# Kernel tuning notes

Hardware: AMD Instinct MI355X
Metric: run time of the kernel (lower is better)

The kernel has to match this reference:

```python
import jax, jax.numpy as jnp
import numpy as np

B_GRAPHS = 32
EMB = 512
ESM = 1280
HEADS = 8
HEAD_DIM = EMB // HEADS


def _segments():
    lengths = 256 + 8 * np.arange(B_GRAPHS)          # 256..504, N = 12160
    batch_ids = np.repeat(np.arange(B_GRAPHS), lengths).astype(np.int32)
    pos = np.concatenate([np.arange(l) for l in lengths]).astype(np.int32)
    return batch_ids, pos, int(lengths.max()), int(lengths.sum())


def setup_inputs() -> dict:
    key = jax.random.key(0)
    ks = jax.random.split(key, 10)
    batch_ids, pos, pad_len, n = _segments()
    s = 0.02
    return {
        "esm_embedding": jax.random.normal(ks[0], (n, ESM), jnp.float32),
        "h": jax.random.normal(ks[1], (n, EMB), jnp.float32),
        "W_esm": jax.random.normal(ks[2], (EMB, ESM), jnp.float32) * s,
        "b_esm": jnp.zeros((EMB,), jnp.float32),
        "Wq": jax.random.normal(ks[3], (EMB, EMB), jnp.float32) * s,
        "bq": jnp.zeros((EMB,), jnp.float32),
        "Wk": jax.random.normal(ks[4], (EMB, EMB), jnp.float32) * s,
        "bk": jnp.zeros((EMB,), jnp.float32),
        "Wv": jax.random.normal(ks[5], (EMB, EMB), jnp.float32) * s,
        "bv": jnp.zeros((EMB,), jnp.float32),
        "Wo": jax.random.normal(ks[6], (EMB, EMB), jnp.float32) * s,
        "bo": jnp.zeros((EMB,), jnp.float32),
        "gamma": jnp.ones((EMB,), jnp.float32),
        "beta": jnp.zeros((EMB,), jnp.float32),
        "batch_ids": jnp.asarray(batch_ids),
        "pos": jnp.asarray(pos),
        "pad_len": pad_len,
        "num_graphs": B_GRAPHS,
    }


def _layer_norm(x, gamma, beta, eps=1e-5):
    mu = jnp.mean(x, axis=-1, keepdims=True)
    var = jnp.var(x, axis=-1, keepdims=True)
    return (x - mu) * jax.lax.rsqrt(var + eps) * gamma + beta


def reference(esm_embedding, h, W_esm, b_esm, Wq, bq, Wk, bk, Wv, bv, Wo, bo,
              gamma, beta, batch_ids, pos, pad_len, num_graphs):
    B, P, D, H, hd = num_graphs, pad_len, EMB, HEADS, HEAD_DIM
    residual = h
    # to_dense_batch: scatter nodes into [B, P, *] padded tensors + key mask
    h_dense = jnp.zeros((B, P, D), h.dtype).at[batch_ids, pos].set(h)
    h_mask = jnp.zeros((B, P), bool).at[batch_ids, pos].set(True)
    h_esm = esm_embedding @ W_esm.T + b_esm                      # [N, D]
    esm_dense = jnp.zeros((B, P, D), h.dtype).at[batch_ids, pos].set(h_esm)

    q = (h_dense @ Wq.T + bq).reshape(B, P, H, hd)
    k = (esm_dense @ Wk.T + bk).reshape(B, P, H, hd)
    v = (esm_dense @ Wv.T + bv).reshape(B, P, H, hd)

    scores = jnp.einsum("bqhd,bkhd->bhqk", q, k) / jnp.sqrt(jnp.float32(hd))
    scores = jnp.where(h_mask[:, None, None, :], scores, -jnp.inf)
    attn = jax.nn.softmax(scores, axis=-1)                        # [B,H,P,P]
    out = jnp.einsum("bhqk,bkhd->bqhd", attn, v).reshape(B, P, D)
    out = out @ Wo.T + bo
    out = out[batch_ids, pos]                                     # unpad -> [N, D]
    return _layer_norm(out + residual, gamma, beta)
```

## Files before the change

### kernel.cpp

```cpp
#include <hip/hip_runtime.h>

#define NTOT 12160
#define EMBD 512
#define ESMD 1280
#define NHEAD 8
#define HD 64
#define NG 32
#define NTILE 768

typedef __attribute__((ext_vector_type(8))) short short8v;
typedef __attribute__((ext_vector_type(4))) short short4v;
typedef __attribute__((ext_vector_type(4))) float floatx4;

__device__ inline short f2bf(float f) {
  union { float f; unsigned u; } v; v.f = f;
  unsigned r = v.u + 0x7fffu + ((v.u >> 16) & 1u);
  return (short)(r >> 16);
}

__device__ inline void gload_lds16(const void* g, void* l) {
  __builtin_amdgcn_global_load_lds((const __attribute__((address_space(1))) void*)g,
                                   (__attribute__((address_space(3))) void*)l, 16, 0, 0);
}

__device__ inline int node_graph(int n) {
  int g = (int)((sqrtf(3969.f + (float)n) - 63.f) * 0.5f);
  if (4 * (g + 1) * (g + 64) <= n) g++;
  else if (4 * g * (g + 63) > n) g--;
  return g;
}

__global__ __launch_bounds__(256) void cvt_kernel(
    const float* __restrict__ esm, const float* __restrict__ Wq,
    const float* __restrict__ Wk, const float* __restrict__ Wv,
    const float* __restrict__ Wo,
    short* __restrict__ esm_b, short* __restrict__ Wq_b,
    short* __restrict__ Wk_b, short* __restrict__ Wv_b, short* __restrict__ Wo_b)
{
  int idx = blockIdx.x * 256 + threadIdx.x;
  const float* src; short* dst; int off;
  if      (idx < 3891200) { src = esm; dst = esm_b; off = idx; }
  else if (idx < 3956736) { src = Wq;  dst = Wq_b;  off = idx - 3891200; }
  else if (idx < 4022272) { src = Wk;  dst = Wk_b;  off = idx - 3956736; }
  else if (idx < 4087808) { src = Wv;  dst = Wv_b;  off = idx - 4022272; }
  else                    { src = Wo;  dst = Wo_b;  off = idx - 4087808; }
  const float4 v = *(const float4*)&src[(size_t)off * 4];
  short4v s; s[0] = f2bf(v.x); s[1] = f2bf(v.y); s[2] = f2bf(v.z); s[3] = f2bf(v.w);
  *(short4v*)&dst[(size_t)off * 4] = s;
}

__global__ __launch_bounds__(256) void wtrans_kernel(
    const float* __restrict__ W, short* __restrict__ WT)
{
  __shared__ short t[32][33];
  const int c0 = blockIdx.x * 32;
  const int r0 = blockIdx.y * 32;
  const int tr = threadIdx.x >> 5, tc = threadIdx.x & 31;
  for (int i = 0; i < 4; i++)
    t[i * 8 + tr][tc] = f2bf(W[(size_t)(r0 + i * 8 + tr) * 1280 + c0 + tc]);
  __syncthreads();
  for (int i = 0; i < 4; i++)
    WT[(size_t)(c0 + i * 8 + tr) * 512 + r0 + tc] = t[tc][i * 8 + tr];
}

__global__ __launch_bounds__(256) void bfuse_kernel(
    const float* __restrict__ Wk, const float* __restrict__ Wv,
    const float* __restrict__ besm, const float* __restrict__ bk,
    const float* __restrict__ bv, float* __restrict__ bkp, float* __restrict__ bvp)
{
  int wgid = blockIdx.x * 4 + (threadIdx.x >> 6);
  int lane = threadIdx.x & 63;
  const float* W  = (wgid < 512) ? Wk : Wv;
  const float* ba = (wgid < 512) ? bk : bv;
  float* o        = (wgid < 512) ? bkp : bvp;
  int row = wgid & 511;
  const float4 w0 = *(const float4*)&W[(size_t)row * 512 + lane * 8];
  const float4 w1 = *(const float4*)&W[(size_t)row * 512 + lane * 8 + 4];
  const float4 b0 = *(const float4*)&besm[lane * 8];
  const float4 b1 = *(const float4*)&besm[lane * 8 + 4];
  float s = w0.x * b0.x + w0.y * b0.y + w0.z * b0.z + w0.w * b0.w
          + w1.x * b1.x + w1.y * b1.y + w1.z * b1.z + w1.w * b1.w;
  for (int off = 1; off < 64; off <<= 1) s += __shfl_xor(s, off);
  if (lane == 0) o[row] = s + ba[row];
}

template<int AF32>
__device__ inline void gemm_core(const void* __restrict__ Ap, const short* __restrict__ W,
                                 int K, int row0, int col0,
                                 short* As, short* Bs, floatx4 acc[4][4])
{
  const int tid = threadIdx.x;
  const int lane = tid & 63, wave = tid >> 6;
  const int l15 = lane & 15, quad = lane >> 4;
  const int wm = (wave >> 1) * 64, wn = (wave & 1) * 64;
  const int lrow = lane >> 3;
  const int scol = ((lane & 7) ^ lrow) * 8;
  const int swz = l15 & 7;

  for (int k0 = 0; k0 < K; k0 += 64) {
    if (k0) __syncthreads();
    if (AF32) {
      const float* A = (const float*)Ap;
      for (int p = 0; p < 8; p++) {
        int idx = p * 256 + tid;
        int r = idx >> 4, c4 = idx & 15;
        const float4 v = *(const float4*)&A[(size_t)(row0 + r) * K + k0 + c4 * 4];
        short4v sv; sv[0] = f2bf(v.x); sv[1] = f2bf(v.y); sv[2] = f2bf(v.z); sv[3] = f2bf(v.w);
        *(short4v*)&As[r * 64 + (((c4 >> 1) ^ (r & 7)) << 3) + ((c4 & 1) << 2)] = sv;
      }
    } else {
      const short* A = (const short*)Ap;
      for (int p = 0; p < 4; p++) {
        int seg = wave * 4 + p;
        gload_lds16(&A[(size_t)(row0 + seg * 8 + lrow) * K + k0 + scol], &As[seg * 512]);
      }
    }
    for (int p = 0; p < 4; p++) {
      int seg = wave * 4 + p;
      gload_lds16(&W[(size_t)(col0 + seg * 8 + lrow) * K + k0 + scol], &Bs[seg * 512]);
    }
    __syncthreads();
    for (int ks = 0; ks < 64; ks += 32) {
      const int off = (((ks >> 3) + quad) ^ swz) << 3;
      short8v a[4], b[4];
      for (int mt = 0; mt < 4; mt++)
        a[mt] = *(const short8v*)&As[(wm + mt * 16 + l15) * 64 + off];
      for (int nt = 0; nt < 4; nt++)
        b[nt] = *(const short8v*)&Bs[(wn + nt * 16 + l15) * 64 + off];
      for (int mt = 0; mt < 4; mt++)
        for (int nt = 0; nt < 4; nt++)
          acc[mt][nt] = __builtin_amdgcn_mfma_f32_16x16x32_bf16(a[mt], b[nt], acc[mt][nt], 0, 0, 0);
    }
  }
}

__device__ inline void epi_bf16(floatx4 acc[4][4], const float* bias, short* C,
                                int row0, int col0, int wm, int wn, int l15, int quad)
{
  for (int nt = 0; nt < 4; nt++) {
    int col = col0 + wn + nt * 16 + l15;
    float bv = bias[col];
    for (int mt = 0; mt < 4; mt++) {
      int rowb = row0 + wm + mt * 16 + quad * 4;
      for (int r = 0; r < 4; r++)
        C[(size_t)(rowb + r) * EMBD + col] = f2bf(acc[mt][nt][r] + bv);
    }
  }
}

__global__ __launch_bounds__(256) void wfuse_gemm(
    const short* __restrict__ Wk_b, const short* __restrict__ Wv_b,
    const short* __restrict__ WT, short* __restrict__ Wkp, short* __restrict__ Wvp)
{
  __shared__ short As[128 * 64];
  __shared__ short Bs[128 * 64];
  const int wh = blockIdx.x >= 10;
  const int col0 = (blockIdx.x - (wh ? 10 : 0)) * 128;
  const int row0 = blockIdx.y * 128;
  floatx4 acc[4][4];
  for (int i = 0; i < 4; i++) for (int j = 0; j < 4; j++)
    for (int r = 0; r < 4; r++) acc[i][j][r] = 0.f;
  gemm_core<0>(wh ? Wv_b : Wk_b, WT, 512, row0, col0, As, Bs, acc);
  short* O = wh ? Wvp : Wkp;
  const int lane = threadIdx.x & 63, wave = threadIdx.x >> 6;
  const int l15 = lane & 15, quad = lane >> 4;
  const int wm = (wave >> 1) * 64, wn = (wave & 1) * 64;
  for (int nt = 0; nt < 4; nt++) {
    int col = col0 + wn + nt * 16 + l15;
    for (int mt = 0; mt < 4; mt++) {
      int rowb = row0 + wm + mt * 16 + quad * 4;
      for (int r = 0; r < 4; r++)
        O[(size_t)(rowb + r) * ESMD + col] = f2bf(acc[mt][nt][r]);
    }
  }
}

__global__ __launch_bounds__(256) void qkv_gemm(
    const float* __restrict__ hf, const short* __restrict__ esm_b,
    const short* __restrict__ Wq_b, const short* __restrict__ Wkp, const short* __restrict__ Wvp,
    const float* __restrict__ bq, const float* __restrict__ bkp, const float* __restrict__ bvp,
    short* __restrict__ qb, short* __restrict__ kp, short* __restrict__ vp)
{
  __shared__ short As[128 * 64];
  __shared__ short Bs[128 * 64];
  const int which = blockIdx.x >> 2;
  const int row0 = blockIdx.y * 128, col0 = (blockIdx.x & 3) * 128;
  floatx4 acc[4][4];
  for (int i = 0; i < 4; i++) for (int j = 0; j < 4; j++)
    for (int r = 0; r < 4; r++) acc[i][j][r] = 0.f;
  if (which == 0) gemm_core<1>(hf,    Wq_b, 512,  row0, col0, As, Bs, acc);
  else if (which == 1) gemm_core<0>(esm_b, Wkp, 1280, row0, col0, As, Bs, acc);
  else gemm_core<0>(esm_b, Wvp, 1280, row0, col0, As, Bs, acc);

  const int lane = threadIdx.x & 63, wave = threadIdx.x >> 6;
  const int l15 = lane & 15, quad = lane >> 4;
  const int wm = (wave >> 1) * 64, wn = (wave & 1) * 64;

  if (which == 0) {
    epi_bf16(acc, bq, qb, row0, col0, wm, wn, l15, quad);
  } else if (which == 1) {
    for (int mt = 0; mt < 4; mt++) {
      int rowb = row0 + wm + mt * 16 + quad * 4;
      int g = node_graph(rowb);
      int loc = rowb - 4 * g * (g + 63);
      int ptile = 16 * g + (g * g) / 4 + (loc >> 4);
      int l15k = loc & 15;
      for (int nt = 0; nt < 4; nt++) {
        int col = col0 + wn + nt * 16 + l15;
        float bv = bkp[col];
        int hh = col >> 6, dh = col & 63;
        int hfh = dh >> 5, qk = (dh & 31) >> 3, jk = dh & 7;
        size_t base = ((size_t)(hh * NTILE + ptile) * 2 + hfh) * 512
                      + (size_t)l15k * 32 + qk * 8 + jk;
        for (int r = 0; r < 4; r++)
          kp[base + (size_t)r * 32] = f2bf(acc[mt][nt][r] + bv);
      }
    }
  } else {
    for (int mt = 0; mt < 4; mt++) {
      int rowb = row0 + wm + mt * 16 + quad * 4;
      int g = node_graph(rowb);
      int loc = rowb - 4 * g * (g + 63);
      int ptile = 16 * g + (g * g) / 4 + (loc >> 4);
      int koff = loc & 15;
      for (int nt = 0; nt < 4; nt++) {
        int col = col0 + wn + nt * 16 + l15;
        float bv = bvp[col];
        int hh = col >> 6, dh = col & 63;
        int dt = dh >> 4, l15v = dh & 15;
        size_t base = ((size_t)(hh * 4 + dt) * NTILE + ptile) * 256
                      + (size_t)l15v * 16 + koff;
        short4v sv;
        for (int r = 0; r < 4; r++) sv[r] = f2bf(acc[mt][nt][r] + bv);
        *(short4v*)&vp[base] = sv;
      }
    }
  }
}

template<bool MASK>
__device__ inline void attn_chunk(
    int kc, int L, int Tg, int hb, int hdt4,
    const short* __restrict__ kp, const short* __restrict__ vp,
    short* Ps, const short8v& aq0, const short8v& aq1,
    floatx4 oacc[4], float rowsum[4], int l15, int quad)
{
  floatx4 s[4];
  const int t0 = Tg + (kc >> 4);
  for (int sub = 0; sub < 4; sub++) {
    const short* kpt = &kp[((size_t)(hb + t0 + sub) * 2) * 512 + l15 * 32 + quad * 8];
    short8v b0 = *(const short8v*)kpt;
    short8v b1 = *(const short8v*)(kpt + 512);
    floatx4 c; for (int r = 0; r < 4; r++) c[r] = 0.f;
    c = __builtin_amdgcn_mfma_f32_16x16x32_bf16(aq0, b0, c, 0, 0, 0);
    c = __builtin_amdgcn_mfma_f32_16x16x32_bf16(aq1, b1, c, 0, 0, 0);
    s[sub] = c;
  }
  for (int sub = 0; sub < 4; sub++)
    for (int r = 0; r < 4; r++) {
      float p = __expf(s[sub][r] * 0.125f);
      if (MASK && (kc + sub * 16 + l15 >= L)) p = 0.f;
      rowsum[r] += p;
      Ps[(quad * 4 + r) * 72 + sub * 16 + l15] = f2bf(p);
    }
  for (int half = 0; half < 2; half++) {
    short8v pA = *(const short8v*)&Ps[l15 * 72 + half * 32 + quad * 8];
    for (int dt = 0; dt < 4; dt++) {
      size_t vbase = ((size_t)(hdt4 + dt) * NTILE + t0 + half * 2 + (quad >> 1)) * 256
                     + (size_t)l15 * 16 + (quad & 1) * 8;
      short8v bvv = *(const short8v*)&vp[vbase];
      oacc[dt] = __builtin_amdgcn_mfma_f32_16x16x32_bf16(pA, bvv, oacc[dt], 0, 0, 0);
    }
  }
}

__global__ __launch_bounds__(512) void attn_kernel(
    const short* __restrict__ qb, const short* __restrict__ kp,
    const short* __restrict__ vp, short* __restrict__ ao)
{
  __shared__ short Ps_all[8][16 * 72];
  const int x = blockIdx.x & 7, j = blockIdx.x >> 3;
  int g = -1, qt = 0, accum = 0;
  for (int i = 0; i < 4; i++) {
    int gg = x + 8 * i;
    int t = 16 + ((gg + 1) >> 1);
    if (j < accum + t) { g = gg; qt = j - accum; break; }
    accum += t;
  }
  if (g < 0) return;
  const int L = 256 + 8 * g;
  const int start = 4 * g * (g + 63);
  const int Tg = 16 * g + (g * g) / 4;
  const int h = threadIdx.x >> 6;
  const int lane = threadIdx.x & 63;
  const int l15 = lane & 15, quad = lane >> 4;
  const int hb = h * NTILE, hdt4 = h * 4;
  short* Ps = Ps_all[h];

  int qrow = qt * 16 + l15;
  if (qrow > L - 1) qrow = L - 1;
  const size_t qoff = (size_t)(start + qrow) * EMBD + h * HD + quad * 8;
  const short8v aq0 = *(const short8v*)&qb[qoff];
  const short8v aq1 = *(const short8v*)&qb[qoff + 32];

  float rowsum[4];
  floatx4 oacc[4];
  for (int r = 0; r < 4; r++) rowsum[r] = 0.f;
  for (int dt = 0; dt < 4; dt++)
    for (int r = 0; r < 4; r++) oacc[dt][r] = 0.f;

  const int Lfull = L & ~63;
  for (int kc = 0; kc < Lfull; kc += 64)
    attn_chunk<false>(kc, L, Tg, hb, hdt4, kp, vp, Ps, aq0, aq1, oacc, rowsum, l15, quad);
  if (Lfull < L)
    attn_chunk<true>(Lfull, L, Tg, hb, hdt4, kp, vp, Ps, aq0, aq1, oacc, rowsum, l15, quad);

  float inv[4];
  for (int r = 0; r < 4; r++) {
    float red = rowsum[r];
    red += __shfl_xor(red, 1); red += __shfl_xor(red, 2);
    red += __shfl_xor(red, 4); red += __shfl_xor(red, 8);
    inv[r] = 1.f / red;
  }
  for (int dt = 0; dt < 4; dt++)
    for (int r = 0; r < 4; r++) {
      int rl = qt * 16 + quad * 4 + r;
      if (rl < L)
        ao[(size_t)(start + rl) * EMBD + h * HD + dt * 16 + l15] = f2bf(oacc[dt][r] * inv[r]);
    }
}

__global__ __launch_bounds__(256) void o_gemm(
    const short* __restrict__ A, const short* __restrict__ W,
    const float* __restrict__ bias, float* __restrict__ C)
{
  __shared__ short As[128 * 64];
  __shared__ short Bs[128 * 64];
  floatx4 acc[4][4];
  for (int i = 0; i < 4; i++) for (int j = 0; j < 4; j++)
    for (int r = 0; r < 4; r++) acc[i][j][r] = 0.f;
  const int row0 = blockIdx.y * 128, col0 = blockIdx.x * 128;
  gemm_core<0>(A, W, EMBD, row0, col0, As, Bs, acc);
  const int lane = threadIdx.x & 63, wave = threadIdx.x >> 6;
  const int l15 = lane & 15, quad = lane >> 4;
  const int wm = (wave >> 1) * 64, wn = (wave & 1) * 64;
  for (int nt = 0; nt < 4; nt++) {
    int col = col0 + wn + nt * 16 + l15;
    float bv = bias[col];
    for (int mt = 0; mt < 4; mt++) {
      int rowb = row0 + wm + mt * 16 + quad * 4;
      for (int r = 0; r < 4; r++)
        C[(size_t)(rowb + r) * EMBD + col] = acc[mt][nt][r] + bv;
    }
  }
}

__global__ __launch_bounds__(64) void ln_kernel(
    float* __restrict__ y, const float* __restrict__ hres,
    const float* __restrict__ gamma, const float* __restrict__ beta)
{
  const int row = blockIdx.x;
  const int lane = threadIdx.x;
  const size_t base = (size_t)row * EMBD + lane * 8;
  const float4 a0 = *(const float4*)&y[base];
  const float4 a1 = *(const float4*)&y[base + 4];
  const float4 b0 = *(const float4*)&hres[base];
  const float4 b1 = *(const float4*)&hres[base + 4];
  float x[8] = { a0.x + b0.x, a0.y + b0.y, a0.z + b0.z, a0.w + b0.w,
                 a1.x + b1.x, a1.y + b1.y, a1.z + b1.z, a1.w + b1.w };
  float s = 0.f, s2 = 0.f;
  for (int i = 0; i < 8; i++) { s += x[i]; s2 += x[i] * x[i]; }
  for (int off = 1; off < 64; off <<= 1) { s += __shfl_xor(s, off); s2 += __shfl_xor(s2, off); }
  const float mu = s * (1.f / 512.f);
  const float var = s2 * (1.f / 512.f) - mu * mu;
  const float rstd = rsqrtf(var + 1e-5f);
  const float4 g0 = *(const float4*)&gamma[lane * 8];
  const float4 g1 = *(const float4*)&gamma[lane * 8 + 4];
  const float4 e0 = *(const float4*)&beta[lane * 8];
  const float4 e1 = *(const float4*)&beta[lane * 8 + 4];
  const float gg[8] = { g0.x, g0.y, g0.z, g0.w, g1.x, g1.y, g1.z, g1.w };
  const float ee[8] = { e0.x, e0.y, e0.z, e0.w, e1.x, e1.y, e1.z, e1.w };
  float o[8];
  for (int i = 0; i < 8; i++) o[i] = (x[i] - mu) * rstd * gg[i] + ee[i];
  *(float4*)&y[base]     = make_float4(o[0], o[1], o[2], o[3]);
  *(float4*)&y[base + 4] = make_float4(o[4], o[5], o[6], o[7]);
}

extern "C" void kernel_launch(void* const* d_in, const int* in_sizes, int n_in,
                              void* d_out, int out_size, void* d_ws, size_t ws_size,
                              hipStream_t stream)
{
  (void)in_sizes; (void)n_in; (void)out_size; (void)ws_size;
  const float* esm   = (const float*)d_in[0];
  const float* h     = (const float*)d_in[1];
  const float* Wesm  = (const float*)d_in[2];
  const float* besm  = (const float*)d_in[3];
  const float* Wq    = (const float*)d_in[4];
  const float* bq    = (const float*)d_in[5];
  const float* Wk    = (const float*)d_in[6];
  const float* bk    = (const float*)d_in[7];
  const float* Wv    = (const float*)d_in[8];
  const float* bv    = (const float*)d_in[9];
  const float* Wo    = (const float*)d_in[10];
  const float* bo    = (const float*)d_in[11];
  const float* gamma = (const float*)d_in[12];
  const float* beta  = (const float*)d_in[13];

  char* ws = (char*)d_ws;
  short* esm_b  = (short*)ws;
  short* ao     = esm_b;
  short* kp     = (short*)(ws + 31129600);
  short* WesmT  = kp;
  short* vp     = (short*)(ws + 43712512);
  short* Wq_b   = (short*)(ws + 56295424);
  short* Wk_b   = (short*)(ws + 56819712);
  short* Wv_b   = (short*)(ws + 57344000);
  short* Wo_b   = (short*)(ws + 57868288);
  short* Wkp    = (short*)(ws + 58392576);
  short* Wvp    = (short*)(ws + 59703296);
  float* bkp    = (float*)(ws + 61014016);
  float* bvp    = (float*)(ws + 61016064);
  short* qb     = (short*)d_out;
  float* y      = (float*)d_out;

  cvt_kernel<<<dim3(16224), dim3(256), 0, stream>>>(
      esm, Wq, Wk, Wv, Wo, esm_b, Wq_b, Wk_b, Wv_b, Wo_b);
  wtrans_kernel<<<dim3(40, 16), dim3(256), 0, stream>>>(Wesm, WesmT);
  bfuse_kernel<<<dim3(256), dim3(256), 0, stream>>>(Wk, Wv, besm, bk, bv, bkp, bvp);
  wfuse_gemm<<<dim3(20, 4), dim3(256), 0, stream>>>(Wk_b, Wv_b, WesmT, Wkp, Wvp);
  qkv_gemm<<<dim3(12, 95), dim3(256), 0, stream>>>(
      h, esm_b, Wq_b, Wkp, Wvp, bq, bkp, bvp, qb, kp, vp);
  attn_kernel<<<dim3(832), dim3(512), 0, stream>>>(qb, kp, vp, ao);
  o_gemm<<<dim3(4, 95), dim3(256), 0, stream>>>(ao, Wo_b, bo, y);
  ln_kernel<<<dim3(NTOT), dim3(64), 0, stream>>>(y, h, gamma, beta);
}
```

Measured before the change: 306.6 us.

## Widen QKV GEMM tile to 128x256, pre-convert h to bf16, XCD-aware block mapping

The h input is converted to bf16 in the bulk conversion kernel and written into spare space in the output buffer, so the QKV GEMM loads both operands through direct global-to-LDS copies instead of an fp32 load-convert path. The QKV GEMM becomes a 512-thread block with a 128x256 output tile, which halves the number of times each A row tile is re-read. A 1D grid is remapped so that blocks sharing a row tile land on the same XCD, to improve L2 reuse of A. The trade-offs are an extra conversion pass over h, a larger LDS footprint per block, and some idle blocks past the last row tile.

```diff
diff --git a/kernel.cpp b/kernel.cpp
--- a/kernel.cpp
+++ b/kernel.cpp
@@ -31,19 +31,20 @@
 }
 
 __global__ __launch_bounds__(256) void cvt_kernel(
-    const float* __restrict__ esm, const float* __restrict__ Wq,
-    const float* __restrict__ Wk, const float* __restrict__ Wv,
-    const float* __restrict__ Wo,
-    short* __restrict__ esm_b, short* __restrict__ Wq_b,
+    const float* __restrict__ esm, const float* __restrict__ h,
+    const float* __restrict__ Wq, const float* __restrict__ Wk,
+    const float* __restrict__ Wv, const float* __restrict__ Wo,
+    short* __restrict__ esm_b, short* __restrict__ h_b, short* __restrict__ Wq_b,
     short* __restrict__ Wk_b, short* __restrict__ Wv_b, short* __restrict__ Wo_b)
 {
   int idx = blockIdx.x * 256 + threadIdx.x;
   const float* src; short* dst; int off;
   if      (idx < 3891200) { src = esm; dst = esm_b; off = idx; }
-  else if (idx < 3956736) { src = Wq;  dst = Wq_b;  off = idx - 3891200; }
-  else if (idx < 4022272) { src = Wk;  dst = Wk_b;  off = idx - 3956736; }
-  else if (idx < 4087808) { src = Wv;  dst = Wv_b;  off = idx - 4022272; }
-  else                    { src = Wo;  dst = Wo_b;  off = idx - 4087808; }
+  else if (idx < 5447680) { src = h;   dst = h_b;   off = idx - 3891200; }
+  else if (idx < 5513216) { src = Wq;  dst = Wq_b;  off = idx - 5447680; }
+  else if (idx < 5578752) { src = Wk;  dst = Wk_b;  off = idx - 5513216; }
+  else if (idx < 5644288) { src = Wv;  dst = Wv_b;  off = idx - 5578752; }
+  else                    { src = Wo;  dst = Wo_b;  off = idx - 5644288; }
   const float4 v = *(const float4*)&src[(size_t)off * 4];
   short4v s; s[0] = f2bf(v.x); s[1] = f2bf(v.y); s[2] = f2bf(v.z); s[3] = f2bf(v.w);
   *(short4v*)&dst[(size_t)off * 4] = s;
@@ -84,8 +85,7 @@
   if (lane == 0) o[row] = s + ba[row];
 }
 
-template<int AF32>
-__device__ inline void gemm_core(const void* __restrict__ Ap, const short* __restrict__ W,
+__device__ inline void gemm_core(const short* __restrict__ A, const short* __restrict__ W,
                                  int K, int row0, int col0,
                                  short* As, short* Bs, floatx4 acc[4][4])
 {
@@ -99,21 +99,9 @@
 
   for (int k0 = 0; k0 < K; k0 += 64) {
     if (k0) __syncthreads();
-    if (AF32) {
-      const float* A = (const float*)Ap;
-      for (int p = 0; p < 8; p++) {
-        int idx = p * 256 + tid;
-        int r = idx >> 4, c4 = idx & 15;
-        const float4 v = *(const float4*)&A[(size_t)(row0 + r) * K + k0 + c4 * 4];
-        short4v sv; sv[0] = f2bf(v.x); sv[1] = f2bf(v.y); sv[2] = f2bf(v.z); sv[3] = f2bf(v.w);
-        *(short4v*)&As[r * 64 + (((c4 >> 1) ^ (r & 7)) << 3) + ((c4 & 1) << 2)] = sv;
-      }
-    } else {
-      const short* A = (const short*)Ap;
-      for (int p = 0; p < 4; p++) {
-        int seg = wave * 4 + p;
-        gload_lds16(&A[(size_t)(row0 + seg * 8 + lrow) * K + k0 + scol], &As[seg * 512]);
-      }
+    for (int p = 0; p < 4; p++) {
+      int seg = wave * 4 + p;
+      gload_lds16(&A[(size_t)(row0 + seg * 8 + lrow) * K + k0 + scol], &As[seg * 512]);
     }
     for (int p = 0; p < 4; p++) {
       int seg = wave * 4 + p;
@@ -160,7 +148,7 @@
   floatx4 acc[4][4];
   for (int i = 0; i < 4; i++) for (int j = 0; j < 4; j++)
     for (int r = 0; r < 4; r++) acc[i][j][r] = 0.f;
-  gemm_core<0>(wh ? Wv_b : Wk_b, WT, 512, row0, col0, As, Bs, acc);
+  gemm_core(wh ? Wv_b : Wk_b, WT, 512, row0, col0, As, Bs, acc);
   short* O = wh ? Wvp : Wkp;
   const int lane = threadIdx.x & 63, wave = threadIdx.x >> 6;
   const int l15 = lane & 15, quad = lane >> 4;
@@ -175,26 +163,61 @@
   }
 }
 
-__global__ __launch_bounds__(256) void qkv_gemm(
-    const float* __restrict__ hf, const short* __restrict__ esm_b,
+__global__ __launch_bounds__(512) void qkv_gemm(
+    const short* __restrict__ hb, const short* __restrict__ esm_b,
     const short* __restrict__ Wq_b, const short* __restrict__ Wkp, const short* __restrict__ Wvp,
     const float* __restrict__ bq, const float* __restrict__ bkp, const float* __restrict__ bvp,
     short* __restrict__ qb, short* __restrict__ kp, short* __restrict__ vp)
 {
   __shared__ short As[128 * 64];
-  __shared__ short Bs[128 * 64];
-  const int which = blockIdx.x >> 2;
-  const int row0 = blockIdx.y * 128, col0 = (blockIdx.x & 3) * 128;
+  __shared__ short Bs[256 * 64];
+  const int bid = blockIdx.x;
+  const int xcd = bid & 7, idx = bid >> 3;
+  const int rowc = idx / 6, c = idx - rowc * 6;
+  const int r = xcd + 8 * rowc;
+  if (r >= 95) return;
+  const int row0 = r * 128;
+  const int col0 = (c & 1) * 256;
+  const int which = c >> 1;
+  const short* A = (which == 0) ? hb : esm_b;
+  const short* W = (which == 0) ? Wq_b : (which == 1 ? Wkp : Wvp);
+  const int K = (which == 0) ? 512 : 1280;
+
+  const int tid = threadIdx.x;
+  const int lane = tid & 63, wave = tid >> 6;
+  const int l15 = lane & 15, quad = lane >> 4;
+  const int wm = (wave >> 2) * 64, wn = (wave & 3) * 64;
+  const int lrow = lane >> 3;
+  const int scol = ((lane & 7) ^ lrow) * 8;
+  const int swz = l15 & 7;
+
   floatx4 acc[4][4];
   for (int i = 0; i < 4; i++) for (int j = 0; j < 4; j++)
-    for (int r = 0; r < 4; r++) acc[i][j][r] = 0.f;
-  if (which == 0) gemm_core<1>(hf,    Wq_b, 512,  row0, col0, As, Bs, acc);
-  else if (which == 1) gemm_core<0>(esm_b, Wkp, 1280, row0, col0, As, Bs, acc);
-  else gemm_core<0>(esm_b, Wvp, 1280, row0, col0, As, Bs, acc);
-
-  const int lane = threadIdx.x & 63, wave = threadIdx.x >> 6;
-  const int l15 = lane & 15, quad = lane >> 4;
-  const int wm = (wave >> 1) * 64, wn = (wave & 1) * 64;
+    for (int rr = 0; rr < 4; rr++) acc[i][j][rr] = 0.f;
+
+  for (int k0 = 0; k0 < K; k0 += 64) {
+    if (k0) __syncthreads();
+    for (int p = 0; p < 2; p++) {
+      int seg = wave * 2 + p;
+      gload_lds16(&A[(size_t)(row0 + seg * 8 + lrow) * K + k0 + scol], &As[seg * 512]);
+    }
+    for (int p = 0; p < 4; p++) {
+      int seg = wave * 4 + p;
+      gload_lds16(&W[(size_t)(col0 + seg * 8 + lrow) * K + k0 + scol], &Bs[seg * 512]);
+    }
+    __syncthreads();
+    for (int ks = 0; ks < 64; ks += 32) {
+      const int off = (((ks >> 3) + quad) ^ swz) << 3;
+      short8v a[4], b[4];
+      for (int mt = 0; mt < 4; mt++)
+        a[mt] = *(const short8v*)&As[(wm + mt * 16 + l15) * 64 + off];
+      for (int nt = 0; nt < 4; nt++)
+        b[nt] = *(const short8v*)&Bs[(wn + nt * 16 + l15) * 64 + off];
+      for (int mt = 0; mt < 4; mt++)
+        for (int nt = 0; nt < 4; nt++)
+          acc[mt][nt] = __builtin_amdgcn_mfma_f32_16x16x32_bf16(a[mt], b[nt], acc[mt][nt], 0, 0, 0);
+    }
+  }
 
   if (which == 0) {
     epi_bf16(acc, bq, qb, row0, col0, wm, wn, l15, quad);
@@ -212,8 +235,8 @@
         int hfh = dh >> 5, qk = (dh & 31) >> 3, jk = dh & 7;
         size_t base = ((size_t)(hh * NTILE + ptile) * 2 + hfh) * 512
                       + (size_t)l15k * 32 + qk * 8 + jk;
-        for (int r = 0; r < 4; r++)
-          kp[base + (size_t)r * 32] = f2bf(acc[mt][nt][r] + bv);
+        for (int rr = 0; rr < 4; rr++)
+          kp[base + (size_t)rr * 32] = f2bf(acc[mt][nt][rr] + bv);
       }
     }
   } else {
@@ -231,7 +254,7 @@
         size_t base = ((size_t)(hh * 4 + dt) * NTILE + ptile) * 256
                       + (size_t)l15v * 16 + koff;
         short4v sv;
-        for (int r = 0; r < 4; r++) sv[r] = f2bf(acc[mt][nt][r] + bv);
+        for (int rr = 0; rr < 4; rr++) sv[rr] = f2bf(acc[mt][nt][rr] + bv);
         *(short4v*)&vp[base] = sv;
       }
     }
@@ -340,7 +363,7 @@
   for (int i = 0; i < 4; i++) for (int j = 0; j < 4; j++)
     for (int r = 0; r < 4; r++) acc[i][j][r] = 0.f;
   const int row0 = blockIdx.y * 128, col0 = blockIdx.x * 128;
-  gemm_core<0>(A, W, EMBD, row0, col0, As, Bs, acc);
+  gemm_core(A, W, EMBD, row0, col0, As, Bs, acc);
   const int lane = threadIdx.x & 63, wave = threadIdx.x >> 6;
   const int l15 = lane & 15, quad = lane >> 4;
   const int wm = (wave >> 1) * 64, wn = (wave & 1) * 64;
@@ -421,15 +444,16 @@
   float* bkp    = (float*)(ws + 61014016);
   float* bvp    = (float*)(ws + 61016064);
   short* qb     = (short*)d_out;
+  short* h_b    = (short*)((char*)d_out + 12451840);
   float* y      = (float*)d_out;
 
-  cvt_kernel<<<dim3(16224), dim3(256), 0, stream>>>(
-      esm, Wq, Wk, Wv, Wo, esm_b, Wq_b, Wk_b, Wv_b, Wo_b);
+  cvt_kernel<<<dim3(22304), dim3(256), 0, stream>>>(
+      esm, h, Wq, Wk, Wv, Wo, esm_b, h_b, Wq_b, Wk_b, Wv_b, Wo_b);
   wtrans_kernel<<<dim3(40, 16), dim3(256), 0, stream>>>(Wesm, WesmT);
   bfuse_kernel<<<dim3(256), dim3(256), 0, stream>>>(Wk, Wv, besm, bk, bv, bkp, bvp);
   wfuse_gemm<<<dim3(20, 4), dim3(256), 0, stream>>>(Wk_b, Wv_b, WesmT, Wkp, Wvp);
-  qkv_gemm<<<dim3(12, 95), dim3(256), 0, stream>>>(
-      h, esm_b, Wq_b, Wkp, Wvp, bq, bkp, bvp, qb, kp, vp);
+  qkv_gemm<<<dim3(576), dim3(512), 0, stream>>>(
+      h_b, esm_b, Wq_b, Wkp, Wvp, bq, bkp, bvp, qb, kp, vp);
   attn_kernel<<<dim3(832), dim3(512), 0, stream>>>(qb, kp, vp, ao);
   o_gemm<<<dim3(4, 95), dim3(256), 0, stream>>>(ao, Wo_b, bo, y);
   ln_kernel<<<dim3(NTOT), dim3(64), 0, stream>>>(y, h, gamma, beta);
```

After: 309.0 us. Within noise of the previous version (+0.8%).
